# Performance work log

Measured on AMD Instinct MI355X. Metric: run time of the kernel, lower is better.

## Reference

```python
import jax, jax.numpy as jnp
import numpy as np

NOISE_LEVEL = 0.05  # midpoint of uniform(0.01, 0.1) in the original
A_COEF = 0.99
B_COEF = 0.01


def setup_inputs() -> dict:
    key = jax.random.key(0)
    k1, k2 = jax.random.split(key)
    C, T = 256, 220500
    waveform = jax.random.normal(k1, (C, T), dtype=jnp.float32)
    white_noise = jax.random.normal(k2, (C, T), dtype=jnp.float32)
    return {"waveform": waveform, "white_noise": white_noise}


def _pink_noise(white_noise):
    # First-order IIR: f[0] = w[0]; f[i] = 0.99*f[i-1] + 0.01*w[i]
    # Vectorized over channels, lax.scan over time.
    w0 = white_noise[:, 0]                      # [C]
    wt = white_noise[:, 1:].T                   # [T-1, C]

    def step(carry, w_t):
        f = A_COEF * carry + B_COEF * w_t
        return f, f

    _, rest = jax.lax.scan(step, w0, wt)        # rest: [T-1, C]
    pink = jnp.concatenate([w0[None, :], rest], axis=0).T  # [C, T]
    return pink


def reference(waveform, white_noise):
    pink = _pink_noise(white_noise)
    mixed = waveform + pink * NOISE_LEVEL
    max_val = jnp.max(jnp.abs(mixed))
    # normalize only if peak exceeds 1.0
    return jnp.where(max_val > 1.0, mixed / max_val, mixed)
```

## Files before the change

### kernel.cpp

```cpp
#include <hip/hip_runtime.h>


#define TLEN 220500
#define CHANNELS 256

constexpr int CL   = 8192;
constexpr int NT   = 256;
constexpr int NSB  = 8;
constexpr int NCHUNK = (TLEN + CL - 1) / CL;
constexpr int NBLK = NCHUNK * CHANNELS;

constexpr float AC = 0.99f;
constexpr float BC = 0.01f;
constexpr float NL = 0.05f;

constexpr double dpow(double a, int n) { double r = 1.0; for (int i = 0; i < n; ++i) r *= a; return r; }

constexpr float WP0 = (float)dpow(0.99, 4 * 1);
constexpr float WP1 = (float)dpow(0.99, 4 * 2);
constexpr float WP2 = (float)dpow(0.99, 4 * 4);
constexpr float WP3 = (float)dpow(0.99, 4 * 8);
constexpr float WP4 = (float)dpow(0.99, 4 * 16);
constexpr float WP5 = (float)dpow(0.99, 4 * 32);
constexpr float A256  = (float)dpow(0.99, 256);
constexpr float A1024 = (float)dpow(0.99, 1024);
constexpr float L2A4   = -0.05799827878044602f;
constexpr float L2A256 = -3.7118898419485456f;

__global__ void init_max_kernel(unsigned int* gmax) { *gmax = 0u; }

__device__ __forceinline__ float wave_scan4(float f, int lane) {
    { float o = __shfl_up(f, 1,  64); if (lane >= 1)  f = fmaf(WP0, o, f); }
    { float o = __shfl_up(f, 2,  64); if (lane >= 2)  f = fmaf(WP1, o, f); }
    { float o = __shfl_up(f, 4,  64); if (lane >= 4)  f = fmaf(WP2, o, f); }
    { float o = __shfl_up(f, 8,  64); if (lane >= 8)  f = fmaf(WP3, o, f); }
    { float o = __shfl_up(f, 16, 64); if (lane >= 16) f = fmaf(WP4, o, f); }
    { float o = __shfl_up(f, 32, 64); if (lane >= 32) f = fmaf(WP5, o, f); }
    return f;
}

#define PIN4(v) asm volatile("" : "+v"((v).x), "+v"((v).y), "+v"((v).z), "+v"((v).w))

template <int USE_ATOMIC>
__global__ __launch_bounds__(NT, 2)
void pink_mix_kernel(const float* __restrict__ waveform,
                     const float* __restrict__ white,
                     float* __restrict__ out,
                     unsigned int* __restrict__ gmax,
                     float* __restrict__ blockmax)
{
    __shared__ float sB[NSB + 1][4];
    __shared__ float sM[4];
    __shared__ float sW0;

    const int chunk = blockIdx.x;
    const int ch    = blockIdx.y;
    const int c0    = chunk * CL;
    const size_t rowoff = (size_t)ch * TLEN;
    const float* __restrict__ wrow = white + rowoff;
    const float* __restrict__ arow = waveform + rowoff;
    float* __restrict__ orow = out + rowoff;

    const int tid  = threadIdx.x;
    const int lane = tid & 63;
    const int wv   = tid >> 6;

    float4 wf[NSB];
    float4 af[NSB];
    #pragma unroll
    for (int i = 0; i < NSB; ++i) {
        int g = c0 + i * 1024 + 4 * tid;
        if (g < TLEN) {
            wf[i] = *reinterpret_cast<const float4*>(wrow + g);
            af[i] = *reinterpret_cast<const float4*>(arow + g);
        } else {
            wf[i] = make_float4(0.f, 0.f, 0.f, 0.f);
            af[i] = make_float4(0.f, 0.f, 0.f, 0.f);
        }
    }
    float4 wu = make_float4(0.f, 0.f, 0.f, 0.f);
    if (chunk > 0)
        wu = *reinterpret_cast<const float4*>(wrow + (c0 - 1024) + 4 * tid);
    #pragma unroll
    for (int i = 0; i < NSB; ++i) { PIN4(wf[i]); PIN4(af[i]); }
    PIN4(wu);

    float eB[NSB];
    #pragma unroll
    for (int i = 0; i < NSB; ++i) {
        float f = BC * wf[i].x;
        f = fmaf(AC, f, BC * wf[i].y);
        f = fmaf(AC, f, BC * wf[i].z);
        f = fmaf(AC, f, BC * wf[i].w);
        float pB = wave_scan4(f, lane);
        float e  = __shfl_up(pB, 1, 64);
        eB[i] = (lane == 0) ? 0.f : e;
        if (lane == 63) sB[i][wv] = pB;
    }

    if (chunk > 0) {
        float f = BC * wu.x;
        f = fmaf(AC, f, BC * wu.y);
        f = fmaf(AC, f, BC * wu.z);
        f = fmaf(AC, f, BC * wu.w);
        float pB = wave_scan4(f, lane);
        if (lane == 63) sB[NSB][wv] = pB;
    }
    if (tid == 0) sW0 = wf[0].x;
    __syncthreads();

    float E;
    if (chunk > 0) {
        float t = sB[NSB][0];
        t = fmaf(A256, t, sB[NSB][1]);
        t = fmaf(A256, t, sB[NSB][2]);
        t = fmaf(A256, t, sB[NSB][3]);
        E = t;
    } else {
        E = sW0;
    }

    const float D4L = __builtin_exp2f((float)lane * L2A4);
    const float DW  = __builtin_exp2f((float)wv   * L2A256);

    float mx = 0.f;
    #pragma unroll
    for (int i = 0; i < NSB; ++i) {
        const float b0 = sB[i][0], b1 = sB[i][1], b2 = sB[i][2];
        float wB = 0.f;
        if (wv > 0) wB = b0;
        if (wv > 1) wB = fmaf(A256, wB, b1);
        if (wv > 2) wB = fmaf(A256, wB, b2);
        float f = fmaf(D4L, fmaf(DW, E, wB), eB[i]);

        int g = c0 + i * 1024 + 4 * tid;
        if (g < TLEN) {
            float4 m;
            f = fmaf(AC, f, BC * wf[i].x); m.x = fmaf(NL, f, af[i].x);
            f = fmaf(AC, f, BC * wf[i].y); m.y = fmaf(NL, f, af[i].y);
            f = fmaf(AC, f, BC * wf[i].z); m.z = fmaf(NL, f, af[i].z);
            f = fmaf(AC, f, BC * wf[i].w); m.w = fmaf(NL, f, af[i].w);
            *reinterpret_cast<float4*>(orow + g) = m;
            mx = fmaxf(mx, fmaxf(fmaxf(fabsf(m.x), fabsf(m.y)),
                                 fmaxf(fabsf(m.z), fabsf(m.w))));
        }
        float t = b0;
        t = fmaf(A256, t, b1);
        t = fmaf(A256, t, b2);
        t = fmaf(A256, t, sB[i][3]);
        E = fmaf(A1024, E, t);
    }

    #pragma unroll
    for (int d = 32; d >= 1; d >>= 1)
        mx = fmaxf(mx, __shfl_xor(mx, d, 64));
    if (lane == 0) sM[wv] = mx;
    __syncthreads();
    if (tid == 0) {
        float m = fmaxf(fmaxf(sM[0], sM[1]), fmaxf(sM[2], sM[3]));
        if (USE_ATOMIC) {
            atomicMax(gmax, __float_as_uint(m));
        } else {
            blockmax[ch * NCHUNK + chunk] = m;
        }
    }
}

__global__ __launch_bounds__(256)
void reduce_max_kernel(const float* __restrict__ blockmax, unsigned int* __restrict__ gmax)
{
    __shared__ float sM[4];
    const int tid  = threadIdx.x;
    const int lane = tid & 63;
    const int wv   = tid >> 6;
    float mx = 0.f;
    for (int i = tid; i < NBLK; i += 256)
        mx = fmaxf(mx, blockmax[i]);
    #pragma unroll
    for (int d = 32; d >= 1; d >>= 1)
        mx = fmaxf(mx, __shfl_xor(mx, d, 64));
    if (lane == 0) sM[wv] = mx;
    __syncthreads();
    if (tid == 0)
        *gmax = __float_as_uint(fmaxf(fmaxf(sM[0], sM[1]), fmaxf(sM[2], sM[3])));
}

__global__ __launch_bounds__(256)
void scale_kernel(float* __restrict__ out, const unsigned int* __restrict__ gmax, int n4)
{
    const float m = __uint_as_float(*gmax);
    const float s = (m > 1.0f) ? (1.0f / m) : 1.0f;
    float4* p = reinterpret_cast<float4*>(out);
    int i = blockIdx.x * blockDim.x + threadIdx.x;
    const int stride = gridDim.x * blockDim.x;
    for (; i < n4; i += stride) {
        float4 v = p[i];
        v.x *= s; v.y *= s; v.z *= s; v.w *= s;
        p[i] = v;
    }
}

extern "C" void kernel_launch(void* const* d_in, const int* in_sizes, int n_in,
                              void* d_out, int out_size, void* d_ws, size_t ws_size,
                              hipStream_t stream)
{
    const float* waveform = (const float*)d_in[0];
    const float* white    = (const float*)d_in[1];
    float* out            = (float*)d_out;

    unsigned int* gmax = (unsigned int*)d_ws;
    float* blockmax    = (float*)((char*)d_ws + 256);
    const bool ws_ok   = ws_size >= 256 + (size_t)NBLK * sizeof(float);

    dim3 grid(NCHUNK, CHANNELS);
    const int n4 = out_size / 4;

    if (ws_ok) {
        hipLaunchKernelGGL((pink_mix_kernel<0>), grid, dim3(NT), 0, stream,
                           waveform, white, out, gmax, blockmax);
        hipLaunchKernelGGL(reduce_max_kernel, dim3(1), dim3(256), 0, stream,
                           blockmax, gmax);
    } else {
        hipLaunchKernelGGL(init_max_kernel, dim3(1), dim3(1), 0, stream, gmax);
        hipLaunchKernelGGL((pink_mix_kernel<1>), grid, dim3(NT), 0, stream,
                           waveform, white, out, gmax, blockmax);
    }
    hipLaunchKernelGGL(scale_kernel, dim3(3072), dim3(256), 0, stream,
                       out, gmax, n4);
}
```

Measured before the change: 232.1 us.

## Process nine chunks per block with double-buffered register prefetch

Each block now walks nine consecutive 8192-sample chunks of a channel instead of one. It carries the IIR state forward in-register, so only the first chunk needs the lookback from the previous 1024 samples. The next chunk's loads are issued into a second register buffer while the current one is scanned, which overlaps memory with compute. In exchange the grid drops from 6912 to 768 blocks and register use doubles, which may lower occupancy or cause spills under launch_bounds(256,2).

```diff
diff --git a/kernel.cpp b/kernel.cpp
--- a/kernel.cpp
+++ b/kernel.cpp
@@ -7,8 +7,10 @@
 constexpr int CL   = 8192;
 constexpr int NT   = 256;
 constexpr int NSB  = 8;
-constexpr int NCHUNK = (TLEN + CL - 1) / CL;
-constexpr int NBLK = NCHUNK * CHANNELS;
+constexpr int NCHUNK = 27;
+constexpr int CPB  = 9;
+constexpr int BPC  = NCHUNK / CPB;
+constexpr int NBLK = BPC * CHANNELS;
 
 constexpr float AC = 0.99f;
 constexpr float BC = 0.01f;
@@ -41,6 +43,27 @@
 
 #define PIN4(v) asm volatile("" : "+v"((v).x), "+v"((v).y), "+v"((v).z), "+v"((v).w))
 
+struct ChunkBuf { float4 wf[NSB]; float4 af[NSB]; };
+
+__device__ __forceinline__ void load_chunk(const float* __restrict__ wrow,
+                                           const float* __restrict__ arow,
+                                           int c0, int tid, ChunkBuf& b)
+{
+    #pragma unroll
+    for (int i = 0; i < NSB; ++i) {
+        int g = c0 + i * 1024 + 4 * tid;
+        if (g < TLEN) {
+            b.wf[i] = *reinterpret_cast<const float4*>(wrow + g);
+            b.af[i] = *reinterpret_cast<const float4*>(arow + g);
+        } else {
+            b.wf[i] = make_float4(0.f, 0.f, 0.f, 0.f);
+            b.af[i] = make_float4(0.f, 0.f, 0.f, 0.f);
+        }
+    }
+    #pragma unroll
+    for (int i = 0; i < NSB; ++i) { PIN4(b.wf[i]); PIN4(b.af[i]); }
+}
+
 template <int USE_ATOMIC>
 __global__ __launch_bounds__(NT, 2)
 void pink_mix_kernel(const float* __restrict__ waveform,
@@ -53,9 +76,9 @@
     __shared__ float sM[4];
     __shared__ float sW0;
 
-    const int chunk = blockIdx.x;
+    const int bx    = blockIdx.x;
     const int ch    = blockIdx.y;
-    const int c0    = chunk * CL;
+    const int cbase = bx * CPB * CL;
     const size_t rowoff = (size_t)ch * TLEN;
     const float* __restrict__ wrow = white + rowoff;
     const float* __restrict__ arow = waveform + rowoff;
@@ -65,90 +88,93 @@
     const int lane = tid & 63;
     const int wv   = tid >> 6;
 
-    float4 wf[NSB];
-    float4 af[NSB];
-    #pragma unroll
-    for (int i = 0; i < NSB; ++i) {
-        int g = c0 + i * 1024 + 4 * tid;
-        if (g < TLEN) {
-            wf[i] = *reinterpret_cast<const float4*>(wrow + g);
-            af[i] = *reinterpret_cast<const float4*>(arow + g);
-        } else {
-            wf[i] = make_float4(0.f, 0.f, 0.f, 0.f);
-            af[i] = make_float4(0.f, 0.f, 0.f, 0.f);
-        }
-    }
-    float4 wu = make_float4(0.f, 0.f, 0.f, 0.f);
-    if (chunk > 0)
-        wu = *reinterpret_cast<const float4*>(wrow + (c0 - 1024) + 4 * tid);
-    #pragma unroll
-    for (int i = 0; i < NSB; ++i) { PIN4(wf[i]); PIN4(af[i]); }
-    PIN4(wu);
-
-    float eB[NSB];
-    #pragma unroll
-    for (int i = 0; i < NSB; ++i) {
-        float f = BC * wf[i].x;
-        f = fmaf(AC, f, BC * wf[i].y);
-        f = fmaf(AC, f, BC * wf[i].z);
-        f = fmaf(AC, f, BC * wf[i].w);
-        float pB = wave_scan4(f, lane);
-        float e  = __shfl_up(pB, 1, 64);
-        eB[i] = (lane == 0) ? 0.f : e;
-        if (lane == 63) sB[i][wv] = pB;
-    }
-
-    if (chunk > 0) {
-        float f = BC * wu.x;
-        f = fmaf(AC, f, BC * wu.y);
-        f = fmaf(AC, f, BC * wu.z);
-        f = fmaf(AC, f, BC * wu.w);
-        float pB = wave_scan4(f, lane);
-        if (lane == 63) sB[NSB][wv] = pB;
-    }
-    if (tid == 0) sW0 = wf[0].x;
-    __syncthreads();
-
-    float E;
-    if (chunk > 0) {
-        float t = sB[NSB][0];
-        t = fmaf(A256, t, sB[NSB][1]);
-        t = fmaf(A256, t, sB[NSB][2]);
-        t = fmaf(A256, t, sB[NSB][3]);
-        E = t;
-    } else {
-        E = sW0;
-    }
-
     const float D4L = __builtin_exp2f((float)lane * L2A4);
     const float DW  = __builtin_exp2f((float)wv   * L2A256);
 
+    ChunkBuf bA, bB;
+    load_chunk(wrow, arow, cbase, tid, bA);
+    float4 wu = make_float4(0.f, 0.f, 0.f, 0.f);
+    if (bx > 0) {
+        wu = *reinterpret_cast<const float4*>(wrow + (cbase - 1024) + 4 * tid);
+        PIN4(wu);
+    }
+
+    float E  = 0.f;
     float mx = 0.f;
-    #pragma unroll
-    for (int i = 0; i < NSB; ++i) {
-        const float b0 = sB[i][0], b1 = sB[i][1], b2 = sB[i][2];
-        float wB = 0.f;
-        if (wv > 0) wB = b0;
-        if (wv > 1) wB = fmaf(A256, wB, b1);
-        if (wv > 2) wB = fmaf(A256, wB, b2);
-        float f = fmaf(D4L, fmaf(DW, E, wB), eB[i]);
-
-        int g = c0 + i * 1024 + 4 * tid;
-        if (g < TLEN) {
-            float4 m;
-            f = fmaf(AC, f, BC * wf[i].x); m.x = fmaf(NL, f, af[i].x);
-            f = fmaf(AC, f, BC * wf[i].y); m.y = fmaf(NL, f, af[i].y);
-            f = fmaf(AC, f, BC * wf[i].z); m.z = fmaf(NL, f, af[i].z);
-            f = fmaf(AC, f, BC * wf[i].w); m.w = fmaf(NL, f, af[i].w);
-            *reinterpret_cast<float4*>(orow + g) = m;
-            mx = fmaxf(mx, fmaxf(fmaxf(fabsf(m.x), fabsf(m.y)),
-                                 fmaxf(fabsf(m.z), fabsf(m.w))));
-        }
-        float t = b0;
-        t = fmaf(A256, t, b1);
-        t = fmaf(A256, t, b2);
-        t = fmaf(A256, t, sB[i][3]);
-        E = fmaf(A1024, E, t);
+
+    #pragma unroll
+    for (int j = 0; j < CPB; ++j) {
+        const int c0 = cbase + j * CL;
+        ChunkBuf& cur = (j & 1) ? bB : bA;
+        ChunkBuf& nxt = (j & 1) ? bA : bB;
+
+        if (j + 1 < CPB)
+            load_chunk(wrow, arow, c0 + CL, tid, nxt);
+
+        float eB[NSB];
+        #pragma unroll
+        for (int i = 0; i < NSB; ++i) {
+            float f = BC * cur.wf[i].x;
+            f = fmaf(AC, f, BC * cur.wf[i].y);
+            f = fmaf(AC, f, BC * cur.wf[i].z);
+            f = fmaf(AC, f, BC * cur.wf[i].w);
+            float pB = wave_scan4(f, lane);
+            float e  = __shfl_up(pB, 1, 64);
+            eB[i] = (lane == 0) ? 0.f : e;
+            if (lane == 63) sB[i][wv] = pB;
+        }
+        if (j == 0) {
+            if (bx > 0) {
+                float f = BC * wu.x;
+                f = fmaf(AC, f, BC * wu.y);
+                f = fmaf(AC, f, BC * wu.z);
+                f = fmaf(AC, f, BC * wu.w);
+                float pB = wave_scan4(f, lane);
+                if (lane == 63) sB[NSB][wv] = pB;
+            }
+            if (bx == 0 && tid == 0) sW0 = cur.wf[0].x;
+        }
+        __syncthreads();
+
+        if (j == 0) {
+            if (bx > 0) {
+                float t = sB[NSB][0];
+                t = fmaf(A256, t, sB[NSB][1]);
+                t = fmaf(A256, t, sB[NSB][2]);
+                t = fmaf(A256, t, sB[NSB][3]);
+                E = t;
+            } else {
+                E = sW0;
+            }
+        }
+
+        #pragma unroll
+        for (int i = 0; i < NSB; ++i) {
+            const float b0 = sB[i][0], b1 = sB[i][1], b2 = sB[i][2];
+            float wB = 0.f;
+            if (wv > 0) wB = b0;
+            if (wv > 1) wB = fmaf(A256, wB, b1);
+            if (wv > 2) wB = fmaf(A256, wB, b2);
+            float f = fmaf(D4L, fmaf(DW, E, wB), eB[i]);
+
+            int g = c0 + i * 1024 + 4 * tid;
+            if (g < TLEN) {
+                float4 m;
+                f = fmaf(AC, f, BC * cur.wf[i].x); m.x = fmaf(NL, f, cur.af[i].x);
+                f = fmaf(AC, f, BC * cur.wf[i].y); m.y = fmaf(NL, f, cur.af[i].y);
+                f = fmaf(AC, f, BC * cur.wf[i].z); m.z = fmaf(NL, f, cur.af[i].z);
+                f = fmaf(AC, f, BC * cur.wf[i].w); m.w = fmaf(NL, f, cur.af[i].w);
+                *reinterpret_cast<float4*>(orow + g) = m;
+                mx = fmaxf(mx, fmaxf(fmaxf(fabsf(m.x), fabsf(m.y)),
+                                     fmaxf(fabsf(m.z), fabsf(m.w))));
+            }
+            float t = b0;
+            t = fmaf(A256, t, b1);
+            t = fmaf(A256, t, b2);
+            t = fmaf(A256, t, sB[i][3]);
+            E = fmaf(A1024, E, t);
+        }
+        __syncthreads();
     }
 
     #pragma unroll
@@ -161,7 +187,7 @@
         if (USE_ATOMIC) {
             atomicMax(gmax, __float_as_uint(m));
         } else {
-            blockmax[ch * NCHUNK + chunk] = m;
+            blockmax[ch * BPC + bx] = m;
         }
     }
 }
@@ -212,7 +238,7 @@
     float* blockmax    = (float*)((char*)d_ws + 256);
     const bool ws_ok   = ws_size >= 256 + (size_t)NBLK * sizeof(float);
 
-    dim3 grid(NCHUNK, CHANNELS);
+    dim3 grid(BPC, CHANNELS);
     const int n4 = out_size / 4;
 
     if (ws_ok) {
```

Result: slower. 280.7 us (+21.0%).
